# Optimization experiments

Measured on AMD Instinct MI355X. Metric: run time of the kernel, lower is better.

Reference implementation:

```python
import jax, jax.numpy as jnp
import numpy as np

D = 2048       # hidden_size
F = 8192       # intermediate_size
R = 16         # flylora_rank
SCALING = 32.0 / R   # alpha / rank = 2.0
GAMMA = 0.1


def _era(x):
    # ERA(x) = GELU_tanh(x) + gamma * softplus(x)
    return jax.nn.gelu(x, approximate=True) + GAMMA * jax.nn.softplus(x)


def setup_inputs() -> dict:
    key = jax.random.key(0)
    ks = jax.random.split(key, 16)
    s = 0.02
    inp = {
        'x': jax.random.normal(ks[0], (4, 2048, D), dtype=jnp.float32),
        # gate FlyLoRA (weights stored [in, out])
        'Wg':  jax.random.normal(ks[1], (D, F), dtype=jnp.float32) * s,
        'bg':  jnp.zeros((F,), jnp.float32),
        'Wgd': jax.random.normal(ks[2], (D, R), dtype=jnp.float32) * s,
        'bgd': jnp.zeros((R,), jnp.float32),
        'Wgu': jax.random.normal(ks[3], (R, F), dtype=jnp.float32) * s,
        'bgu': jnp.zeros((F,), jnp.float32),
        # up FlyLoRA
        'Wu':  jax.random.normal(ks[4], (D, F), dtype=jnp.float32) * s,
        'bu':  jnp.zeros((F,), jnp.float32),
        'Wud': jax.random.normal(ks[5], (D, R), dtype=jnp.float32) * s,
        'bud': jnp.zeros((R,), jnp.float32),
        'Wuu': jax.random.normal(ks[6], (R, F), dtype=jnp.float32) * s,
        'buu': jnp.zeros((F,), jnp.float32),
        # down_proj
        'Wd':  jax.random.normal(ks[7], (F, D), dtype=jnp.float32) * s,
        'bd':  jnp.zeros((D,), jnp.float32),
    }
    return inp


def _flylora(x, W, b, Wdn, bdn, Wup, bup):
    # base(x) + scaling * lora_up(lora_down(x))
    base = jnp.einsum('bsd,df->bsf', x, W) + b
    lora = jnp.einsum('bsr,rf->bsf', jnp.einsum('bsd,dr->bsr', x, Wdn) + bdn, Wup) + bup
    return base + SCALING * lora


def reference(x, Wg, bg, Wgd, bgd, Wgu, bgu, Wu, bu, Wud, bud, Wuu, buu, Wd, bd):
    gate = _era(_flylora(x, Wg, bg, Wgd, bgd, Wgu, bgu))
    up = _flylora(x, Wu, bu, Wud, bud, Wuu, buu)
    return jnp.einsum('bsf,fd->bsd', gate * up, Wd) + bd
```

## Files before the change

### kernel.cpp

```cpp
#include <hip/hip_runtime.h>
#include <cstdint>
#include <cstddef>

#define D_DIM 2048
#define F_DIM 8192
#define M_DIM 8192
#define SCALING 2.0f
#define GAMMA 0.1f
#define BUFE 4096

typedef __bf16 bf16x8 __attribute__((ext_vector_type(8)));
typedef float f32x4 __attribute__((ext_vector_type(4)));
typedef unsigned short ushort_t;

#define VMCNT(n) asm volatile("s_waitcnt vmcnt(" #n ")" ::: "memory")

__device__ __forceinline__ unsigned short f2bf(float f) {
  unsigned int u = __float_as_uint(f);
  u += 0x7FFF + ((u >> 16) & 1);
  return (unsigned short)(u >> 16);
}

__device__ __forceinline__ float era_f(float x) {
  float x3 = x * x * x;
  float inner = 0.7978845608028654f * (x + 0.044715f * x3);
  float e = __expf(2.0f * inner);
  float th = 1.0f - 2.0f / (e + 1.0f);
  float gelu = 0.5f * x * (1.0f + th);
  float sp = fmaxf(x, 0.0f) + __logf(1.0f + __expf(-fabsf(x)));
  return gelu + GAMMA * sp;
}


__global__ void convert_x(const float* __restrict__ in, ushort_t* __restrict__ out, int n) {
  int i = (blockIdx.x * 256 + threadIdx.x) * 4;
  if (i >= n) return;
  float4 v = *(const float4*)(in + i);
  out[i + 0] = f2bf(v.x);
  out[i + 1] = f2bf(v.y);
  out[i + 2] = f2bf(v.z);
  out[i + 3] = f2bf(v.w);
}

__global__ void transpose_w(const float* __restrict__ in, ushort_t* __restrict__ out,
                            int K, int N) {
  __shared__ float tile[32][33];
  int k0 = blockIdx.y * 32, n0 = blockIdx.x * 32;
  int tr = threadIdx.x >> 5, tc = threadIdx.x & 31;
#pragma unroll
  for (int i = 0; i < 32; i += 8)
    tile[tr + i][tc] = in[(size_t)(k0 + tr + i) * N + n0 + tc];
  __syncthreads();
#pragma unroll
  for (int i = 0; i < 32; i += 8)
    out[(size_t)(n0 + tr + i) * K + k0 + tc] = f2bf(tile[tc][tr + i]);
}

__global__ void pad_small(const float* __restrict__ in, ushort_t* __restrict__ out, int F) {
  int idx = blockIdx.x * 256 + threadIdx.x;
  int f = idx >> 5, k = idx & 31;
  float v = (k < 16) ? in[(size_t)k * F + f] : 0.0f;
  out[idx] = f2bf(v);
}

__global__ void lora_down(const float* __restrict__ x,
                          const float* __restrict__ Wgd, const float* __restrict__ bgd,
                          const float* __restrict__ Wud, const float* __restrict__ bud,
                          ushort_t* __restrict__ xdg, ushort_t* __restrict__ xdu) {
  int row = blockIdx.x * 8 + (threadIdx.x >> 5);
  int c = threadIdx.x & 31;
  bool isG = (c < 16);
  int col = c & 15;
  const float* W = isG ? Wgd : Wud;
  const float* xr = x + (size_t)row * D_DIM;
  float acc = 0.0f;
  for (int k = 0; k < D_DIM; ++k)
    acc = fmaf(xr[k], W[k * 16 + col], acc);
  float b = isG ? bgd[col] : bud[col];
  ushort_t v = f2bf(SCALING * (acc + b));
  ushort_t* dst = isG ? xdg : xdu;
  dst[row * 32 + col] = v;
  dst[row * 32 + 16 + col] = 0;
}


__device__ __forceinline__ void gload16(const ushort_t* g, ushort_t* l) {
  __builtin_amdgcn_global_load_lds(
      (__attribute__((address_space(1))) void*)g,
      (__attribute__((address_space(3))) void*)l, 16, 0, 0);
}

__device__ __forceinline__ bf16x8 frag_ld(const ushort_t* p) {
  union { uint4 u; bf16x8 v; } un;
  un.u = *(const uint4*)p;
  return un.v;
}


__global__ __launch_bounds__(256, 2) void gemm_gateup(
    const ushort_t* __restrict__ xbf, const ushort_t* __restrict__ Wgt,
    const ushort_t* __restrict__ Wut, const ushort_t* __restrict__ Wgup,
    const ushort_t* __restrict__ Wuup, const ushort_t* __restrict__ xdg,
    const ushort_t* __restrict__ xdu,
    const float* __restrict__ bg, const float* __restrict__ bgu,
    const float* __restrict__ bu, const float* __restrict__ buu,
    ushort_t* __restrict__ tout) {
  __shared__ __align__(16) ushort_t xs[3 * BUFE];
  __shared__ __align__(16) ushort_t wgs[3 * BUFE];
  __shared__ __align__(16) ushort_t wus[3 * BUFE];
  const int f0 = blockIdx.x * 128;
  const int m0 = blockIdx.y * 128;
  const int t = threadIdx.x;
  const int w = t >> 6, lane = t & 63;
  const int wm = w >> 1, wn = w & 1;
  const int ml = lane & 15, q = lane >> 4;

  const int srow = t >> 2;
  const int csw = ((t & 3) ^ ((srow >> 1) & 3)) * 8;
  const int slotq = (q ^ ((ml >> 1) & 3)) * 8;
  const int dsto = w * 512;

  unsigned int xoff = (unsigned int)(m0 + srow) * D_DIM + csw;
  unsigned int woff = (unsigned int)(f0 + srow) * D_DIM + csw;
  const unsigned int rstep = 64u * D_DIM;
  const unsigned int lmo = (unsigned int)(m0 + srow) * 32 + csw;
  const unsigned int lfo = (unsigned int)(f0 + srow) * 32 + csw;

  auto stage_main = [&](int bi, unsigned int xo, unsigned int wo) {
    ushort_t* xd = xs + bi * BUFE + dsto;
    ushort_t* gd = wgs + bi * BUFE + dsto;
    ushort_t* ud = wus + bi * BUFE + dsto;
    gload16(xbf + xo, xd);  gload16(xbf + xo + rstep, xd + 2048);
    gload16(Wgt + wo, gd);  gload16(Wgt + wo + rstep, gd + 2048);
    gload16(Wut + wo, ud);  gload16(Wut + wo + rstep, ud + 2048);
  };
  auto stage_lora_g = [&](int bi) {
    ushort_t* xd = xs + bi * BUFE + dsto;
    ushort_t* gd = wgs + bi * BUFE + dsto;
    gload16(xdg + lmo, xd);   gload16(xdg + lmo + 2048, xd + 2048);
    gload16(Wgup + lfo, gd);  gload16(Wgup + lfo + 2048, gd + 2048);
  };
  auto stage_lora_u = [&](int bi) {
    ushort_t* xd = xs + bi * BUFE + dsto;
    ushort_t* ud = wus + bi * BUFE + dsto;
    gload16(xdu + lmo, xd);   gload16(xdu + lmo + 2048, xd + 2048);
    gload16(Wuup + lfo, ud);  gload16(Wuup + lfo + 2048, ud + 2048);
  };

  const f32x4 zero4 = {0.f, 0.f, 0.f, 0.f};
  f32x4 accg[4][4], accu[4][4];
#pragma unroll
  for (int i = 0; i < 4; ++i)
#pragma unroll
    for (int j = 0; j < 4; ++j) { accg[i][j] = zero4; accu[i][j] = zero4; }

  auto compute_main = [&](int bi) {
    const ushort_t* xb = xs + bi * BUFE;
    const ushort_t* gb = wgs + bi * BUFE;
    const ushort_t* ub = wus + bi * BUFE;
    bf16x8 af[4], bwf[4];
#pragma unroll
    for (int i = 0; i < 4; ++i) {
      af[i]  = frag_ld(xb + (wm * 64 + i * 16 + ml) * 32 + slotq);
      bwf[i] = frag_ld(gb + (wn * 64 + i * 16 + ml) * 32 + slotq);
    }
#pragma unroll
    for (int mi = 0; mi < 4; ++mi)
#pragma unroll
      for (int ni = 0; ni < 4; ++ni)
        accg[mi][ni] = __builtin_amdgcn_mfma_f32_16x16x32_bf16(af[mi], bwf[ni], accg[mi][ni], 0, 0, 0);
#pragma unroll
    for (int i = 0; i < 4; ++i)
      bwf[i] = frag_ld(ub + (wn * 64 + i * 16 + ml) * 32 + slotq);
#pragma unroll
    for (int mi = 0; mi < 4; ++mi)
#pragma unroll
      for (int ni = 0; ni < 4; ++ni)
        accu[mi][ni] = __builtin_amdgcn_mfma_f32_16x16x32_bf16(af[mi], bwf[ni], accu[mi][ni], 0, 0, 0);
  };
  auto compute_lora_g = [&](int bi) {
    bf16x8 af[4], bwf[4];
#pragma unroll
    for (int i = 0; i < 4; ++i) {
      af[i]  = frag_ld(xs  + bi * BUFE + (wm * 64 + i * 16 + ml) * 32 + slotq);
      bwf[i] = frag_ld(wgs + bi * BUFE + (wn * 64 + i * 16 + ml) * 32 + slotq);
    }
#pragma unroll
    for (int mi = 0; mi < 4; ++mi)
#pragma unroll
      for (int ni = 0; ni < 4; ++ni)
        accg[mi][ni] = __builtin_amdgcn_mfma_f32_16x16x32_bf16(af[mi], bwf[ni], accg[mi][ni], 0, 0, 0);
  };
  auto compute_lora_u = [&](int bi) {
    bf16x8 af[4], bwf[4];
#pragma unroll
    for (int i = 0; i < 4; ++i) {
      af[i]  = frag_ld(xs  + bi * BUFE + (wm * 64 + i * 16 + ml) * 32 + slotq);
      bwf[i] = frag_ld(wus + bi * BUFE + (wn * 64 + i * 16 + ml) * 32 + slotq);
    }
#pragma unroll
    for (int mi = 0; mi < 4; ++mi)
#pragma unroll
      for (int ni = 0; ni < 4; ++ni)
        accu[mi][ni] = __builtin_amdgcn_mfma_f32_16x16x32_bf16(af[mi], bwf[ni], accu[mi][ni], 0, 0, 0);
  };

  stage_main(0, xoff, woff);
  stage_main(1, xoff + 32, woff + 32);
  unsigned int xo_n = xoff + 64, wo_n = woff + 64;

  int bc = 0, bs = 2;
#pragma unroll 1
  for (int kt = 0; kt < 62; ++kt) {
    VMCNT(6);
    __builtin_amdgcn_s_barrier();
    stage_main(bs, xo_n, wo_n);
    xo_n += 32; wo_n += 32;
    compute_main(bc);
    bc = (bc == 2) ? 0 : bc + 1;
    bs = (bs == 2) ? 0 : bs + 1;
  }
  VMCNT(6);
  __builtin_amdgcn_s_barrier();
  stage_lora_g(1);
  compute_main(2);
  VMCNT(4);
  __builtin_amdgcn_s_barrier();
  stage_lora_u(2);
  compute_main(0);
  VMCNT(4);
  __builtin_amdgcn_s_barrier();
  compute_lora_g(1);
  VMCNT(0);
  __builtin_amdgcn_s_barrier();
  compute_lora_u(2);

#pragma unroll
  for (int ni = 0; ni < 4; ++ni) {
    int col = f0 + wn * 64 + ni * 16 + ml;
    float cbg = bg[col] + SCALING * bgu[col];
    float cbu = bu[col] + SCALING * buu[col];
#pragma unroll
    for (int mi = 0; mi < 4; ++mi) {
      int row0 = m0 + wm * 64 + mi * 16 + q * 4;
#pragma unroll
      for (int r = 0; r < 4; ++r) {
        float hg = accg[mi][ni][r] + cbg;
        float hu = accu[mi][ni][r] + cbu;
        tout[(size_t)(row0 + r) * F_DIM + col] = f2bf(era_f(hg) * hu);
      }
    }
  }
}

__global__ __launch_bounds__(256, 2) void gemm_down(
    const ushort_t* __restrict__ tin, const ushort_t* __restrict__ Wdt,
    const float* __restrict__ bd, float* __restrict__ out) {
  __shared__ __align__(16) ushort_t as_[3 * BUFE];
  __shared__ __align__(16) ushort_t bs_[3 * BUFE];
  const int n0 = blockIdx.x * 128;
  const int m0 = blockIdx.y * 128;
  const int t = threadIdx.x;
  const int w = t >> 6, lane = t & 63;
  const int wm = w >> 1, wn = w & 1;
  const int ml = lane & 15, q = lane >> 4;

  const int srow = t >> 2;
  const int csw = ((t & 3) ^ ((srow >> 1) & 3)) * 8;
  const int slotq = (q ^ ((ml >> 1) & 3)) * 8;
  const int dsto = w * 512;

  unsigned int aoff = (unsigned int)(m0 + srow) * F_DIM + csw;
  unsigned int boff = (unsigned int)(n0 + srow) * F_DIM + csw;
  const unsigned int rstep = 64u * F_DIM;

  auto stage = [&](int bi, unsigned int ao, unsigned int bo) {
    ushort_t* ad = as_ + bi * BUFE + dsto;
    ushort_t* bdst = bs_ + bi * BUFE + dsto;
    gload16(tin + ao, ad);   gload16(tin + ao + rstep, ad + 2048);
    gload16(Wdt + bo, bdst); gload16(Wdt + bo + rstep, bdst + 2048);
  };

  const f32x4 zero4 = {0.f, 0.f, 0.f, 0.f};
  f32x4 acc[4][4];
#pragma unroll
  for (int i = 0; i < 4; ++i)
#pragma unroll
    for (int j = 0; j < 4; ++j) acc[i][j] = zero4;

  auto compute = [&](int bi) {
    const ushort_t* ab = as_ + bi * BUFE;
    const ushort_t* bb = bs_ + bi * BUFE;
    bf16x8 af[4], bf_[4];
#pragma unroll
    for (int i = 0; i < 4; ++i) {
      af[i]  = frag_ld(ab + (wm * 64 + i * 16 + ml) * 32 + slotq);
      bf_[i] = frag_ld(bb + (wn * 64 + i * 16 + ml) * 32 + slotq);
    }
#pragma unroll
    for (int mi = 0; mi < 4; ++mi)
#pragma unroll
      for (int ni = 0; ni < 4; ++ni)
        acc[mi][ni] = __builtin_amdgcn_mfma_f32_16x16x32_bf16(af[mi], bf_[ni], acc[mi][ni], 0, 0, 0);
  };

  stage(0, aoff, boff);
  stage(1, aoff + 32, boff + 32);
  unsigned int ao_n = aoff + 64, bo_n = boff + 64;

  const int NT = F_DIM / 32;
  int bc = 0, bsn = 2;
#pragma unroll 1
  for (int kt = 0; kt < NT - 2; ++kt) {
    VMCNT(4);
    __builtin_amdgcn_s_barrier();
    stage(bsn, ao_n, bo_n);
    ao_n += 32; bo_n += 32;
    compute(bc);
    bc = (bc == 2) ? 0 : bc + 1;
    bsn = (bsn == 2) ? 0 : bsn + 1;
  }
  VMCNT(4);
  __builtin_amdgcn_s_barrier();
  compute(2);
  VMCNT(0);
  __builtin_amdgcn_s_barrier();
  compute(0);

#pragma unroll
  for (int ni = 0; ni < 4; ++ni) {
    int col = n0 + wn * 64 + ni * 16 + ml;
    float b = bd[col];
#pragma unroll
    for (int mi = 0; mi < 4; ++mi) {
      int row0 = m0 + wm * 64 + mi * 16 + q * 4;
#pragma unroll
      for (int r = 0; r < 4; ++r)
        out[(size_t)(row0 + r) * D_DIM + col] = acc[mi][ni][r] + b;
    }
  }
}


extern "C" void kernel_launch(void* const* d_in, const int* in_sizes, int n_in,
                              void* d_out, int out_size, void* d_ws, size_t ws_size,
                              hipStream_t stream) {
  const float* x   = (const float*)d_in[0];
  const float* Wg  = (const float*)d_in[1];
  const float* bg  = (const float*)d_in[2];
  const float* Wgd = (const float*)d_in[3];
  const float* bgd = (const float*)d_in[4];
  const float* Wgu = (const float*)d_in[5];
  const float* bgu = (const float*)d_in[6];
  const float* Wu  = (const float*)d_in[7];
  const float* bu  = (const float*)d_in[8];
  const float* Wud = (const float*)d_in[9];
  const float* bud = (const float*)d_in[10];
  const float* Wuu = (const float*)d_in[11];
  const float* buu = (const float*)d_in[12];
  const float* Wd  = (const float*)d_in[13];
  const float* bd  = (const float*)d_in[14];
  float* out = (float*)d_out;

  char* ws = (char*)d_ws;
  size_t off = 0;
  auto alloc = [&](size_t bytes) {
    char* p = ws + off;
    off += (bytes + 255) & ~(size_t)255;
    return p;
  };
  ushort_t* xbf  = (ushort_t*)alloc((size_t)M_DIM * D_DIM * 2);
  ushort_t* Wgt  = (ushort_t*)alloc((size_t)F_DIM * D_DIM * 2);
  ushort_t* Wut  = (ushort_t*)alloc((size_t)F_DIM * D_DIM * 2);
  ushort_t* Wdt  = (ushort_t*)alloc((size_t)D_DIM * F_DIM * 2);
  ushort_t* Wgup = (ushort_t*)alloc((size_t)F_DIM * 32 * 2);
  ushort_t* Wuup = (ushort_t*)alloc((size_t)F_DIM * 32 * 2);
  ushort_t* xdg  = (ushort_t*)alloc((size_t)M_DIM * 32 * 2);
  ushort_t* xdu  = (ushort_t*)alloc((size_t)M_DIM * 32 * 2);
  ushort_t* tbuf = (ushort_t*)alloc((size_t)M_DIM * F_DIM * 2);

  convert_x<<<(M_DIM * D_DIM / 4 + 255) / 256, 256, 0, stream>>>(x, xbf, M_DIM * D_DIM);
  transpose_w<<<dim3(F_DIM / 32, D_DIM / 32), 256, 0, stream>>>(Wg, Wgt, D_DIM, F_DIM);
  transpose_w<<<dim3(F_DIM / 32, D_DIM / 32), 256, 0, stream>>>(Wu, Wut, D_DIM, F_DIM);
  transpose_w<<<dim3(D_DIM / 32, F_DIM / 32), 256, 0, stream>>>(Wd, Wdt, F_DIM, D_DIM);
  pad_small<<<F_DIM * 32 / 256, 256, 0, stream>>>(Wgu, Wgup, F_DIM);
  pad_small<<<F_DIM * 32 / 256, 256, 0, stream>>>(Wuu, Wuup, F_DIM);
  lora_down<<<M_DIM / 8, 256, 0, stream>>>(x, Wgd, bgd, Wud, bud, xdg, xdu);
  gemm_gateup<<<dim3(F_DIM / 128, M_DIM / 128), 256, 0, stream>>>(
      xbf, Wgt, Wut, Wgup, Wuup, xdg, xdu, bg, bgu, bu, buu, tbuf);
  gemm_down<<<dim3(D_DIM / 128, M_DIM / 128), 256, 0, stream>>>(tbuf, Wdt, bd, out);
}
```

Measured before the change: 1.458 ms.

## Enlarge GEMM block tiles to 512 threads with split-phase loads and MFMA priority

Both GEMMs move from 256-thread 128x128 tiles to 512-thread blocks: gate/up uses 256x128 tiles and down uses 256x256 tiles. Each k-step is split into two phases separated by a barrier, interleaving LDS fragment loads, async global-to-LDS staging and MFMA blocks, with s_setprio raised around the MFMA sections. The larger tiles are meant to raise operand reuse and cut global traffic per FLOP. In exchange, LDS use per block grows, there is an extra barrier per iteration, and the down kernel has more accumulator register pressure, all of which can lower occupancy.

```diff
diff --git a/kernel.cpp b/kernel.cpp
--- a/kernel.cpp
+++ b/kernel.cpp
@@ -7,7 +7,6 @@
 #define M_DIM 8192
 #define SCALING 2.0f
 #define GAMMA 0.1f
-#define BUFE 4096
 
 typedef __bf16 bf16x8 __attribute__((ext_vector_type(8)));
 typedef float f32x4 __attribute__((ext_vector_type(4)));
@@ -97,7 +96,7 @@
 }
 
 
-__global__ __launch_bounds__(256, 2) void gemm_gateup(
+__global__ __launch_bounds__(512, 2) void gemm_gateup(
     const ushort_t* __restrict__ xbf, const ushort_t* __restrict__ Wgt,
     const ushort_t* __restrict__ Wut, const ushort_t* __restrict__ Wgup,
     const ushort_t* __restrict__ Wuup, const ushort_t* __restrict__ xdg,
@@ -105,11 +104,11 @@
     const float* __restrict__ bg, const float* __restrict__ bgu,
     const float* __restrict__ bu, const float* __restrict__ buu,
     ushort_t* __restrict__ tout) {
-  __shared__ __align__(16) ushort_t xs[3 * BUFE];
-  __shared__ __align__(16) ushort_t wgs[3 * BUFE];
-  __shared__ __align__(16) ushort_t wus[3 * BUFE];
+  __shared__ __align__(16) ushort_t lA[3 * 8192];
+  __shared__ __align__(16) ushort_t lBg[3 * 4096];
+  __shared__ __align__(16) ushort_t lBu[3 * 4096];
   const int f0 = blockIdx.x * 128;
-  const int m0 = blockIdx.y * 128;
+  const int m0 = blockIdx.y * 256;
   const int t = threadIdx.x;
   const int w = t >> 6, lane = t & 63;
   const int wm = w >> 1, wn = w & 1;
@@ -118,34 +117,35 @@
   const int srow = t >> 2;
   const int csw = ((t & 3) ^ ((srow >> 1) & 3)) * 8;
   const int slotq = (q ^ ((ml >> 1) & 3)) * 8;
-  const int dsto = w * 512;
+  const int dstw = w * 512;
 
   unsigned int xoff = (unsigned int)(m0 + srow) * D_DIM + csw;
   unsigned int woff = (unsigned int)(f0 + srow) * D_DIM + csw;
-  const unsigned int rstep = 64u * D_DIM;
+  const unsigned int arstep = 128u * D_DIM;
   const unsigned int lmo = (unsigned int)(m0 + srow) * 32 + csw;
   const unsigned int lfo = (unsigned int)(f0 + srow) * 32 + csw;
 
-  auto stage_main = [&](int bi, unsigned int xo, unsigned int wo) {
-    ushort_t* xd = xs + bi * BUFE + dsto;
-    ushort_t* gd = wgs + bi * BUFE + dsto;
-    ushort_t* ud = wus + bi * BUFE + dsto;
-    gload16(xbf + xo, xd);  gload16(xbf + xo + rstep, xd + 2048);
-    gload16(Wgt + wo, gd);  gload16(Wgt + wo + rstep, gd + 2048);
-    gload16(Wut + wo, ud);  gload16(Wut + wo + rstep, ud + 2048);
-  };
-  auto stage_lora_g = [&](int bi) {
-    ushort_t* xd = xs + bi * BUFE + dsto;
-    ushort_t* gd = wgs + bi * BUFE + dsto;
-    gload16(xdg + lmo, xd);   gload16(xdg + lmo + 2048, xd + 2048);
-    gload16(Wgup + lfo, gd);  gload16(Wgup + lfo + 2048, gd + 2048);
-  };
-  auto stage_lora_u = [&](int bi) {
-    ushort_t* xd = xs + bi * BUFE + dsto;
-    ushort_t* ud = wus + bi * BUFE + dsto;
-    gload16(xdu + lmo, xd);   gload16(xdu + lmo + 2048, xd + 2048);
-    gload16(Wuup + lfo, ud);  gload16(Wuup + lfo + 2048, ud + 2048);
-  };
+  auto stageA = [&](int bi, unsigned int ko) {
+    ushort_t* d = lA + bi * 8192 + dstw;
+    gload16(xbf + xoff + ko, d);
+    gload16(xbf + xoff + arstep + ko, d + 4096);
+  };
+  auto stageB = [&](int bi, unsigned int ko) {
+    gload16(Wgt + woff + ko, lBg + bi * 4096 + dstw);
+    gload16(Wut + woff + ko, lBu + bi * 4096 + dstw);
+  };
+  auto stageLoraA_g = [&](int bi) {
+    ushort_t* d = lA + bi * 8192 + dstw;
+    gload16(xdg + lmo, d);
+    gload16(xdg + lmo + 128u * 32, d + 4096);
+  };
+  auto stageLoraB_g = [&](int bi) { gload16(Wgup + lfo, lBg + bi * 4096 + dstw); };
+  auto stageLoraA_u = [&](int bi) {
+    ushort_t* d = lA + bi * 8192 + dstw;
+    gload16(xdu + lmo, d);
+    gload16(xdu + lmo + 128u * 32, d + 4096);
+  };
+  auto stageLoraB_u = [&](int bi) { gload16(Wuup + lfo, lBu + bi * 4096 + dstw); };
 
   const f32x4 zero4 = {0.f, 0.f, 0.f, 0.f};
   f32x4 accg[4][4], accu[4][4];
@@ -154,86 +154,87 @@
 #pragma unroll
     for (int j = 0; j < 4; ++j) { accg[i][j] = zero4; accu[i][j] = zero4; }
 
-  auto compute_main = [&](int bi) {
-    const ushort_t* xb = xs + bi * BUFE;
-    const ushort_t* gb = wgs + bi * BUFE;
-    const ushort_t* ub = wus + bi * BUFE;
-    bf16x8 af[4], bwf[4];
-#pragma unroll
-    for (int i = 0; i < 4; ++i) {
-      af[i]  = frag_ld(xb + (wm * 64 + i * 16 + ml) * 32 + slotq);
-      bwf[i] = frag_ld(gb + (wn * 64 + i * 16 + ml) * 32 + slotq);
-    }
+  bf16x8 af[4], bwf[4];
+  auto loadA = [&](int bi) {
+#pragma unroll
+    for (int i = 0; i < 4; ++i)
+      af[i] = frag_ld(lA + bi * 8192 + (wm * 64 + i * 16 + ml) * 32 + slotq);
+  };
+  auto loadBg = [&](int bi) {
+#pragma unroll
+    for (int i = 0; i < 4; ++i)
+      bwf[i] = frag_ld(lBg + bi * 4096 + (wn * 64 + i * 16 + ml) * 32 + slotq);
+  };
+  auto loadBu = [&](int bi) {
+#pragma unroll
+    for (int i = 0; i < 4; ++i)
+      bwf[i] = frag_ld(lBu + bi * 4096 + (wn * 64 + i * 16 + ml) * 32 + slotq);
+  };
+  auto mfmaG = [&]() {
+    __builtin_amdgcn_s_setprio(1);
 #pragma unroll
     for (int mi = 0; mi < 4; ++mi)
 #pragma unroll
       for (int ni = 0; ni < 4; ++ni)
         accg[mi][ni] = __builtin_amdgcn_mfma_f32_16x16x32_bf16(af[mi], bwf[ni], accg[mi][ni], 0, 0, 0);
-#pragma unroll
-    for (int i = 0; i < 4; ++i)
-      bwf[i] = frag_ld(ub + (wn * 64 + i * 16 + ml) * 32 + slotq);
+    __builtin_amdgcn_s_setprio(0);
+  };
+  auto mfmaU = [&]() {
+    __builtin_amdgcn_s_setprio(1);
 #pragma unroll
     for (int mi = 0; mi < 4; ++mi)
 #pragma unroll
       for (int ni = 0; ni < 4; ++ni)
         accu[mi][ni] = __builtin_amdgcn_mfma_f32_16x16x32_bf16(af[mi], bwf[ni], accu[mi][ni], 0, 0, 0);
-  };
-  auto compute_lora_g = [&](int bi) {
-    bf16x8 af[4], bwf[4];
-#pragma unroll
-    for (int i = 0; i < 4; ++i) {
-      af[i]  = frag_ld(xs  + bi * BUFE + (wm * 64 + i * 16 + ml) * 32 + slotq);
-      bwf[i] = frag_ld(wgs + bi * BUFE + (wn * 64 + i * 16 + ml) * 32 + slotq);
-    }
-#pragma unroll
-    for (int mi = 0; mi < 4; ++mi)
-#pragma unroll
-      for (int ni = 0; ni < 4; ++ni)
-        accg[mi][ni] = __builtin_amdgcn_mfma_f32_16x16x32_bf16(af[mi], bwf[ni], accg[mi][ni], 0, 0, 0);
-  };
-  auto compute_lora_u = [&](int bi) {
-    bf16x8 af[4], bwf[4];
-#pragma unroll
-    for (int i = 0; i < 4; ++i) {
-      af[i]  = frag_ld(xs  + bi * BUFE + (wm * 64 + i * 16 + ml) * 32 + slotq);
-      bwf[i] = frag_ld(wus + bi * BUFE + (wn * 64 + i * 16 + ml) * 32 + slotq);
-    }
-#pragma unroll
-    for (int mi = 0; mi < 4; ++mi)
-#pragma unroll
-      for (int ni = 0; ni < 4; ++ni)
-        accu[mi][ni] = __builtin_amdgcn_mfma_f32_16x16x32_bf16(af[mi], bwf[ni], accu[mi][ni], 0, 0, 0);
-  };
-
-  stage_main(0, xoff, woff);
-  stage_main(1, xoff + 32, woff + 32);
-  unsigned int xo_n = xoff + 64, wo_n = woff + 64;
+    __builtin_amdgcn_s_setprio(0);
+  };
+
+  stageA(0, 0);  stageB(0, 0);
+  stageA(1, 32); stageB(1, 32);
 
   int bc = 0, bs = 2;
+  unsigned int ko = 64;
 #pragma unroll 1
   for (int kt = 0; kt < 62; ++kt) {
-    VMCNT(6);
+    VMCNT(4);
     __builtin_amdgcn_s_barrier();
-    stage_main(bs, xo_n, wo_n);
-    xo_n += 32; wo_n += 32;
-    compute_main(bc);
+    loadA(bc); loadBg(bc);
+    stageA(bs, ko);
+    mfmaG();
+    __builtin_amdgcn_s_barrier();
+    loadBu(bc);
+    stageB(bs, ko);
+    mfmaU();
+    ko += 32;
     bc = (bc == 2) ? 0 : bc + 1;
     bs = (bs == 2) ? 0 : bs + 1;
   }
-  VMCNT(6);
-  __builtin_amdgcn_s_barrier();
-  stage_lora_g(1);
-  compute_main(2);
   VMCNT(4);
   __builtin_amdgcn_s_barrier();
-  stage_lora_u(2);
-  compute_main(0);
-  VMCNT(4);
-  __builtin_amdgcn_s_barrier();
-  compute_lora_g(1);
+  loadA(2); loadBg(2);
+  stageLoraA_g(1);
+  mfmaG();
+  __builtin_amdgcn_s_barrier();
+  loadBu(2);
+  stageLoraB_g(1);
+  mfmaU();
+  VMCNT(3);
+  __builtin_amdgcn_s_barrier();
+  loadA(0); loadBg(0);
+  stageLoraA_u(2);
+  mfmaG();
+  __builtin_amdgcn_s_barrier();
+  loadBu(0);
+  stageLoraB_u(2);
+  mfmaU();
+  VMCNT(3);
+  __builtin_amdgcn_s_barrier();
+  loadA(1); loadBg(1);
+  mfmaG();
   VMCNT(0);
   __builtin_amdgcn_s_barrier();
-  compute_lora_u(2);
+  loadA(2); loadBu(2);
+  mfmaU();
 
 #pragma unroll
   for (int ni = 0; ni < 4; ++ni) {
@@ -253,13 +254,13 @@
   }
 }
 
-__global__ __launch_bounds__(256, 2) void gemm_down(
+__global__ __launch_bounds__(512, 2) void gemm_down(
     const ushort_t* __restrict__ tin, const ushort_t* __restrict__ Wdt,
     const float* __restrict__ bd, float* __restrict__ out) {
-  __shared__ __align__(16) ushort_t as_[3 * BUFE];
-  __shared__ __align__(16) ushort_t bs_[3 * BUFE];
-  const int n0 = blockIdx.x * 128;
-  const int m0 = blockIdx.y * 128;
+  __shared__ __align__(16) ushort_t lA[3 * 8192];
+  __shared__ __align__(16) ushort_t lB[3 * 8192];
+  const int n0 = blockIdx.x * 256;
+  const int m0 = blockIdx.y * 256;
   const int t = threadIdx.x;
   const int w = t >> 6, lane = t & 63;
   const int wm = w >> 1, wn = w & 1;
@@ -268,68 +269,91 @@
   const int srow = t >> 2;
   const int csw = ((t & 3) ^ ((srow >> 1) & 3)) * 8;
   const int slotq = (q ^ ((ml >> 1) & 3)) * 8;
-  const int dsto = w * 512;
+  const int dstw = w * 512;
 
   unsigned int aoff = (unsigned int)(m0 + srow) * F_DIM + csw;
   unsigned int boff = (unsigned int)(n0 + srow) * F_DIM + csw;
-  const unsigned int rstep = 64u * F_DIM;
-
-  auto stage = [&](int bi, unsigned int ao, unsigned int bo) {
-    ushort_t* ad = as_ + bi * BUFE + dsto;
-    ushort_t* bdst = bs_ + bi * BUFE + dsto;
-    gload16(tin + ao, ad);   gload16(tin + ao + rstep, ad + 2048);
-    gload16(Wdt + bo, bdst); gload16(Wdt + bo + rstep, bdst + 2048);
+  const unsigned int arstep = 128u * F_DIM;
+
+  auto stageA = [&](int bi, unsigned int ko) {
+    ushort_t* d = lA + bi * 8192 + dstw;
+    gload16(tin + aoff + ko, d);
+    gload16(tin + aoff + arstep + ko, d + 4096);
+  };
+  auto stageB = [&](int bi, unsigned int ko) {
+    ushort_t* d = lB + bi * 8192 + dstw;
+    gload16(Wdt + boff + ko, d);
+    gload16(Wdt + boff + arstep + ko, d + 4096);
   };
 
   const f32x4 zero4 = {0.f, 0.f, 0.f, 0.f};
-  f32x4 acc[4][4];
+  f32x4 acc[4][8];
 #pragma unroll
   for (int i = 0; i < 4; ++i)
 #pragma unroll
-    for (int j = 0; j < 4; ++j) acc[i][j] = zero4;
-
-  auto compute = [&](int bi) {
-    const ushort_t* ab = as_ + bi * BUFE;
-    const ushort_t* bb = bs_ + bi * BUFE;
-    bf16x8 af[4], bf_[4];
-#pragma unroll
-    for (int i = 0; i < 4; ++i) {
-      af[i]  = frag_ld(ab + (wm * 64 + i * 16 + ml) * 32 + slotq);
-      bf_[i] = frag_ld(bb + (wn * 64 + i * 16 + ml) * 32 + slotq);
-    }
+    for (int j = 0; j < 8; ++j) acc[i][j] = zero4;
+
+  bf16x8 af[4], bf_[4];
+  auto loadA = [&](int bi) {
+#pragma unroll
+    for (int i = 0; i < 4; ++i)
+      af[i] = frag_ld(lA + bi * 8192 + (wm * 64 + i * 16 + ml) * 32 + slotq);
+  };
+  auto loadB = [&](int bi, int half) {
+#pragma unroll
+    for (int i = 0; i < 4; ++i)
+      bf_[i] = frag_ld(lB + bi * 8192 + (wn * 128 + half * 64 + i * 16 + ml) * 32 + slotq);
+  };
+  auto mfmaH = [&](int half) {
+    __builtin_amdgcn_s_setprio(1);
 #pragma unroll
     for (int mi = 0; mi < 4; ++mi)
 #pragma unroll
       for (int ni = 0; ni < 4; ++ni)
-        acc[mi][ni] = __builtin_amdgcn_mfma_f32_16x16x32_bf16(af[mi], bf_[ni], acc[mi][ni], 0, 0, 0);
-  };
-
-  stage(0, aoff, boff);
-  stage(1, aoff + 32, boff + 32);
-  unsigned int ao_n = aoff + 64, bo_n = boff + 64;
+        acc[mi][half * 4 + ni] =
+            __builtin_amdgcn_mfma_f32_16x16x32_bf16(af[mi], bf_[ni], acc[mi][half * 4 + ni], 0, 0, 0);
+    __builtin_amdgcn_s_setprio(0);
+  };
+
+  stageA(0, 0);  stageB(0, 0);
+  stageA(1, 32); stageB(1, 32);
 
   const int NT = F_DIM / 32;
-  int bc = 0, bsn = 2;
+  int bc = 0, bs = 2;
+  unsigned int ko = 64;
 #pragma unroll 1
   for (int kt = 0; kt < NT - 2; ++kt) {
     VMCNT(4);
     __builtin_amdgcn_s_barrier();
-    stage(bsn, ao_n, bo_n);
-    ao_n += 32; bo_n += 32;
-    compute(bc);
+    loadA(bc); loadB(bc, 0);
+    stageA(bs, ko);
+    mfmaH(0);
+    __builtin_amdgcn_s_barrier();
+    loadB(bc, 1);
+    stageB(bs, ko);
+    mfmaH(1);
+    ko += 32;
     bc = (bc == 2) ? 0 : bc + 1;
-    bsn = (bsn == 2) ? 0 : bsn + 1;
+    bs = (bs == 2) ? 0 : bs + 1;
   }
   VMCNT(4);
   __builtin_amdgcn_s_barrier();
-  compute(2);
+  loadA(bc); loadB(bc, 0);
+  mfmaH(0);
+  __builtin_amdgcn_s_barrier();
+  loadB(bc, 1);
+  mfmaH(1);
+  bc = (bc == 2) ? 0 : bc + 1;
   VMCNT(0);
   __builtin_amdgcn_s_barrier();
-  compute(0);
-
-#pragma unroll
-  for (int ni = 0; ni < 4; ++ni) {
-    int col = n0 + wn * 64 + ni * 16 + ml;
+  loadA(bc); loadB(bc, 0);
+  mfmaH(0);
+  loadB(bc, 1);
+  mfmaH(1);
+
+#pragma unroll
+  for (int ni = 0; ni < 8; ++ni) {
+    int col = n0 + wn * 128 + ni * 16 + ml;
     float b = bd[col];
 #pragma unroll
     for (int mi = 0; mi < 4; ++mi) {
@@ -386,7 +410,7 @@
   pad_small<<<F_DIM * 32 / 256, 256, 0, stream>>>(Wgu, Wgup, F_DIM);
   pad_small<<<F_DIM * 32 / 256, 256, 0, stream>>>(Wuu, Wuup, F_DIM);
   lora_down<<<M_DIM / 8, 256, 0, stream>>>(x, Wgd, bgd, Wud, bud, xdg, xdu);
-  gemm_gateup<<<dim3(F_DIM / 128, M_DIM / 128), 256, 0, stream>>>(
+  gemm_gateup<<<dim3(F_DIM / 128, M_DIM / 256), 512, 0, stream>>>(
       xbf, Wgt, Wut, Wgup, Wuup, xdg, xdu, bg, bgu, bu, buu, tbuf);
-  gemm_down<<<dim3(D_DIM / 128, M_DIM / 128), 256, 0, stream>>>(tbuf, Wdt, bd, out);
-}
+  gemm_down<<<dim3(D_DIM / 256, M_DIM / 256), 512, 0, stream>>>(tbuf, Wdt, bd, out);
+}
```

Result: faster. 1.398 ms (-4.1%).
